# Performance work log

Measured on AMD Instinct MI355X. Metric: run time of the kernel, lower is better.

The kernel has to match this reference:

```python
import jax, jax.numpy as jnp
import numpy as np

IN_FEATURES = 4096
OUT_FEATURES = 4096
BANDWIDTH = min(IN_FEATURES, OUT_FEATURES) // 8  # 512, as in the torch default


def band_indices(n_out, n_in, bw):
    """Vectorized equivalent of BandMatrix.create_band_indices (COO row/col lists)."""
    i = np.arange(n_out)
    lo = np.maximum(0, i - bw)
    hi = np.minimum(n_in, i + bw + 1)
    counts = hi - lo
    total = int(counts.sum())
    rows = np.repeat(i, counts)
    start = np.cumsum(counts) - counts  # offset of each row's first entry
    cols = np.arange(total) - np.repeat(start, counts) + np.repeat(lo, counts)
    return rows.astype(np.int32), cols.astype(np.int32)


def setup_inputs() -> dict:
    key = jax.random.key(0)
    kx, kw = jax.random.split(key)
    rows_np, cols_np = band_indices(OUT_FEATURES, IN_FEATURES, BANDWIDTH)
    nnz = rows_np.shape[0]  # 3935744
    x = jax.random.normal(kx, (4, 2048, IN_FEATURES), dtype=jnp.float32)
    W_values = jax.random.normal(kw, (nnz,), dtype=jnp.float32)
    bias = jnp.zeros((OUT_FEATURES,), dtype=jnp.float32)
    return {
        "x": x,
        "W_values": W_values,
        "bias": bias,
        "rows": jnp.asarray(rows_np),
        "cols": jnp.asarray(cols_np),
    }


def reference(x, W_values, bias, rows, cols):
    # Densify banded COO weight [out, in] (matches sparse_coo_tensor().to_dense()).
    W = jnp.zeros((OUT_FEATURES, IN_FEATURES), dtype=W_values.dtype).at[rows, cols].set(W_values)
    # x: [B, S, in] @ W.T: [in, out] -> [B, S, out]
    out = jnp.einsum('bsi,oi->bso', x, W) + bias
    return out
```

## Files before the change

### kernel.cpp

```cpp
#include <hip/hip_runtime.h>
#include <stdint.h>

#define IN_F  4096
#define OUT_F 4096
#define BW    512
#define WB2   1280
#define BM    256
#define BN    256

typedef __bf16 bf16x8 __attribute__((ext_vector_type(8)));
typedef float  f32x4  __attribute__((ext_vector_type(4)));

__device__ __forceinline__ int band_start(int o) {
    if (o <= 512)  return o * 513 + ((o * (o - 1)) >> 1);
    if (o <= 3584) return 393472 + (o - 512) * 1025;
    const int d = o - 3584;
    return 3542272 + (((1024 + 4609 - o) * d) >> 1);
}

__device__ __forceinline__ uint16_t f32_to_bf16(float f) {
    uint32_t u = __builtin_bit_cast(uint32_t, f);
    u += 0x7FFFu + ((u >> 16) & 1u);
    return (uint16_t)(u >> 16);
}

__global__ __launch_bounds__(256) void cvt_x(const float* __restrict__ x,
                                             uint16_t* __restrict__ xb, int n4) {
    const int stride = gridDim.x * 256;
    for (int i = blockIdx.x * 256 + threadIdx.x; i < n4; i += stride) {
        const float4 v = reinterpret_cast<const float4*>(x)[i];
        const uint32_t lo = (uint32_t)f32_to_bf16(v.x) | ((uint32_t)f32_to_bf16(v.y) << 16);
        const uint32_t hi = (uint32_t)f32_to_bf16(v.z) | ((uint32_t)f32_to_bf16(v.w) << 16);
        reinterpret_cast<uint2*>(xb)[i] = make_uint2(lo, hi);
    }
}

__global__ __launch_bounds__(256) void cvt_w(const float* __restrict__ wv,
                                             uint16_t* __restrict__ wd) {
    const int o = blockIdx.y;
    const int j = blockIdx.x * 256 + threadIdx.x;
    const int i = (o & ~(BM - 1)) - BW + j;
    uint16_t v = 0;
    if (i >= o - BW && i <= o + BW && i >= 0 && i < IN_F) {
        const int lo = (o > BW) ? (o - BW) : 0;
        v = f32_to_bf16(wv[band_start(o) + (i - lo)]);
    }
    wd[o * WB2 + j] = v;
}

__global__ __launch_bounds__(512, 1) void band_gemm_v9(
    const uint16_t* __restrict__ xb,
    const uint16_t* __restrict__ wd,
    const float* __restrict__ bias,
    float* __restrict__ out)
{
    __shared__ __align__(128) uint8_t lds[9 * 16384];

    const int id  = blockIdx.x;
    const int xcd = id & 7;
    const int r   = id >> 3;
    const int bx  = 2 * xcd + (r & 1);
    const int by  = r >> 1;
    const int brow = by * BM;
    const int bcol = bx * BN;

    const int wlo    = bcol - BW;
    const int kstart = wlo > 0 ? wlo : 0;
    const int kend   = (bcol + BN + BW) < IN_F ? (bcol + BN + BW) : IN_F;
    const int nt     = (kend - kstart) >> 6;
    const int j0     = kstart - wlo;

    const int tid  = threadIdx.x;
    const int w    = tid >> 6;
    const int lane = tid & 63;
    const int ln   = lane & 15;
    const int kc   = lane >> 4;
    const int wm   = w >> 2;
    const int wn   = w & 3;

    const int srow = tid >> 3;
    const int csrc = (tid & 7) ^ (srow & 7);
    const uint16_t* aSrc = xb + (size_t)(brow + srow) * IN_F + kstart + csrc * 8;
    const uint16_t* bSrc = wd + (size_t)(bcol + srow) * WB2 + j0 + csrc * 8;

#define GLOAD(srcp, dst_off)                                                             \
    __builtin_amdgcn_global_load_lds(                                                    \
        (const __attribute__((address_space(1))) uint32_t*)(srcp),                       \
        (__attribute__((address_space(3))) uint32_t*)(lds + (dst_off) + (w << 10)),      \
        16, 0, 0)

#define STG_UNIT(w_, j_, slot_) {                                                        \
        if (((j_) & 1) == 0) {                                                           \
            const uint16_t* p_ = aSrc + (size_t)(((j_) >> 1) * 128) * IN_F + (w_) * 64;  \
            GLOAD(p_, (slot_) << 14);                                                    \
            GLOAD(p_ + (size_t)64 * IN_F, ((slot_) << 14) + 8192);                       \
        } else {                                                                         \
            const uint16_t* p_ = bSrc + (size_t)(((j_) >> 1) * 128) * WB2 + (w_) * 64;   \
            GLOAD(p_, (slot_) << 14);                                                    \
            GLOAD(p_ + (size_t)64 * WB2, ((slot_) << 14) + 8192);                        \
        } }

    const int cswz = (kc ^ (ln & 7)) << 4;

#define LD_A(BASE, MQ) {                                                                 \
    _Pragma("unroll")                                                                    \
    for (int s_ = 0; s_ < 4; ++s_) {                                                     \
        const int off_ = (BASE) + (((MQ) * 64 + s_ * 16 + ln) << 7) + cswz;              \
        am[s_][0] = *(const bf16x8*)(lds + off_);                                        \
        am[s_][1] = *(const bf16x8*)(lds + (off_ ^ 64));                                 \
    } }
#define LD_B(DST, BASE, NQ) {                                                            \
    _Pragma("unroll")                                                                    \
    for (int s_ = 0; s_ < 2; ++s_) {                                                     \
        const int off_ = (BASE) + (((wn & 1) * 64 + (NQ) * 32 + s_ * 16 + ln) << 7) + cswz; \
        DST[s_][0] = *(const bf16x8*)(lds + off_);                                       \
        DST[s_][1] = *(const bf16x8*)(lds + (off_ ^ 64));                                \
    } }
#define MFMAPH(MROW, NCOL, BB) {                                                         \
    __builtin_amdgcn_s_setprio(1);                                                       \
    _Pragma("unroll")                                                                    \
    for (int a_ = 0; a_ < 4; ++a_) {                                                     \
        _Pragma("unroll")                                                                \
        for (int n_ = 0; n_ < 2; ++n_) {                                                 \
            acc[(MROW) + a_][(NCOL) + n_] = __builtin_amdgcn_mfma_f32_16x16x32_bf16(     \
                am[a_][0], BB[n_][0], acc[(MROW) + a_][(NCOL) + n_], 0, 0, 0);           \
            acc[(MROW) + a_][(NCOL) + n_] = __builtin_amdgcn_mfma_f32_16x16x32_bf16(     \
                am[a_][1], BB[n_][1], acc[(MROW) + a_][(NCOL) + n_], 0, 0, 0);           \
        } }                                                                              \
    __builtin_amdgcn_s_setprio(0); }

    f32x4 acc[8][4] = {};
    bf16x8 am[4][2], bn0[2][2], bn1[2][2];

    STG_UNIT(0, 0, 0); STG_UNIT(0, 1, 1); STG_UNIT(0, 2, 2); STG_UNIT(0, 3, 3);
    STG_UNIT(1, 0, 4);
    asm volatile("s_waitcnt vmcnt(2)" ::: "memory");
    __builtin_amdgcn_s_barrier();

    int s4v = 0;
    for (int v = 0; v < nt; ++v) {
        int sA = s4v + (wm << 1);           if (sA >= 9) sA -= 9;
        int sB = s4v + 1 + ((wn >> 1) << 1); if (sB >= 9) sB -= 9;
        const int aBase = sA << 14, bBase = sB << 14;
        int st0 = s4v + 5; if (st0 >= 9) st0 -= 9;
        int st1 = st0 + 1; if (st1 >= 9) st1 -= 9;
        int st2 = st1 + 1; if (st2 >= 9) st2 -= 9;
        int st3 = st2 + 1; if (st3 >= 9) st3 -= 9;
        const bool stg_q012 = (v + 1 < nt);
        const bool stg_q3   = (v + 2 < nt);

        LD_A(aBase, 0);
        LD_B(bn0, bBase, 0);
        if (stg_q012) STG_UNIT(v + 1, 1, st0);
        MFMAPH(0, 0, bn0);
        LD_B(bn1, bBase, 1);
        if (stg_q012) STG_UNIT(v + 1, 2, st1);
        MFMAPH(0, 2, bn1);
        LD_A(aBase, 1);
        if (stg_q012) STG_UNIT(v + 1, 3, st2);
        MFMAPH(4, 2, bn1);
        if (stg_q3) STG_UNIT(v + 2, 0, st3);
        MFMAPH(4, 0, bn0);

        if (v + 1 < nt) {
            if (v + 2 < nt) { asm volatile("s_waitcnt vmcnt(2)" ::: "memory"); }
            else            { asm volatile("s_waitcnt vmcnt(0)" ::: "memory"); }
            __builtin_amdgcn_s_barrier();
        }
        s4v += 4; if (s4v >= 9) s4v -= 9;
    }
#undef STG_UNIT
#undef GLOAD

    const int ocol = bcol + wn * 64 + ln;
    float bsv[4];
    #pragma unroll
    for (int n = 0; n < 4; ++n) bsv[n] = bias[ocol + n * 16];

    #pragma unroll
    for (int a = 0; a < 8; ++a) {
        #pragma unroll
        for (int q = 0; q < 4; ++q) {
            const int row = brow + wm * 128 + a * 16 + (kc << 2) + q;
            float* po = out + (size_t)row * OUT_F + ocol;
            #pragma unroll
            for (int n = 0; n < 4; ++n)
                po[n * 16] = acc[a][n][q] + bsv[n];
        }
    }
}

__global__ __launch_bounds__(256) void band_gemm_f32(
    const float* __restrict__ x, const float* __restrict__ wv,
    const float* __restrict__ bias, float* __restrict__ out, int M)
{
    __shared__ float Xs[128][33];
    __shared__ float Ws[32][130];
    const int tid = threadIdx.x;
    const int tx = tid & 15, ty = tid >> 4;
    const int bcol = blockIdx.x * 128, brow = blockIdx.y * 128;
    const int klo = (bcol >= BW) ? (bcol - BW) : 0;
    const int khi = min(IN_F, bcol + 128 + BW);
    float acc[8][8];
    #pragma unroll
    for (int a = 0; a < 8; ++a)
        #pragma unroll
        for (int b = 0; b < 8; ++b) acc[a][b] = 0.f;
    const int xc4 = (tid & 7) * 4, xr0 = tid >> 3;
    const int wc = tid & 31, wr0 = tid >> 5;
    for (int k0 = klo; k0 < khi; k0 += 32) {
        #pragma unroll
        for (int p = 0; p < 4; ++p) {
            const int rr = xr0 + 32 * p;
            const float4 v = *reinterpret_cast<const float4*>(&x[(size_t)(brow + rr) * IN_F + (k0 + xc4)]);
            Xs[rr][xc4 + 0] = v.x; Xs[rr][xc4 + 1] = v.y; Xs[rr][xc4 + 2] = v.z; Xs[rr][xc4 + 3] = v.w;
        }
        const int i = k0 + wc;
        #pragma unroll
        for (int p = 0; p < 16; ++p) {
            const int rr = wr0 + 8 * p;
            const int o = bcol + rr;
            const int lo = (o >= BW) ? (o - BW) : 0;
            float v = 0.f;
            if (i >= o - BW && i <= o + BW) v = wv[band_start(o) + (i - lo)];
            Ws[wc][rr] = v;
        }
        __syncthreads();
        #pragma unroll
        for (int k = 0; k < 32; ++k) {
            float amv[8];
            #pragma unroll
            for (int a = 0; a < 8; ++a) amv[a] = Xs[ty * 8 + a][k];
            float bo[8];
            #pragma unroll
            for (int b = 0; b < 4; ++b) { bo[b] = Ws[k][tx * 4 + b]; bo[4 + b] = Ws[k][tx * 4 + 64 + b]; }
            #pragma unroll
            for (int a = 0; a < 8; ++a)
                #pragma unroll
                for (int b = 0; b < 8; ++b) acc[a][b] = fmaf(amv[a], bo[b], acc[a][b]);
        }
        __syncthreads();
    }
    #pragma unroll
    for (int a = 0; a < 8; ++a) {
        const size_t row = (size_t)(brow + ty * 8 + a);
        #pragma unroll
        for (int b = 0; b < 4; ++b) {
            out[row * OUT_F + bcol + tx * 4 + b]      = acc[a][b]     + bias[bcol + tx * 4 + b];
            out[row * OUT_F + bcol + tx * 4 + 64 + b] = acc[a][4 + b] + bias[bcol + tx * 4 + 64 + b];
        }
    }
}

extern "C" void kernel_launch(void* const* d_in, const int* in_sizes, int n_in,
                              void* d_out, int out_size, void* d_ws, size_t ws_size,
                              hipStream_t stream) {
    const float* x    = (const float*)d_in[0];
    const float* wv   = (const float*)d_in[1];
    const float* bias = (const float*)d_in[2];
    float* out        = (float*)d_out;

    const int M = in_sizes[0] / IN_F;
    const size_t xb_bytes = (size_t)M * IN_F * 2;
    const size_t wd_bytes = (size_t)OUT_F * WB2 * 2;

    if (ws_size >= xb_bytes + wd_bytes && (M % BM) == 0) {
        uint16_t* xb  = (uint16_t*)d_ws;
        uint16_t* wdp = (uint16_t*)((uint8_t*)d_ws + xb_bytes);
        cvt_x<<<2048, 256, 0, stream>>>(x, xb, M * IN_F / 4);
        cvt_w<<<dim3(WB2 / 256, OUT_F), 256, 0, stream>>>(wv, wdp);
        band_gemm_v9<<<(M / BM) * (OUT_F / BN), 512, 0, stream>>>(xb, wdp, bias, out);
    } else {
        dim3 grid(OUT_F / 128, M / 128);
        band_gemm_f32<<<grid, 256, 0, stream>>>(x, wv, bias, out, M);
    }
}
```

Measured before the change: 140.4 us.

## Process two row tiles per block to overlap epilogue with next prologue

The GEMM grid shrinks to 256 persistent-style blocks, and each block computes two 256x256 output tiles (row groups byg and byg+16) in sequence. The second tile's prologue global loads are issued before the first tile's epilogue stores, so the store phase hides load latency and one tail wave is removed. It also drops the s_setprio around MFMA phases. The fast path is now hardcoded to M == 8192, and the kernel does twice the serial work per block.

```diff
diff --git a/kernel.cpp b/kernel.cpp
--- a/kernel.cpp
+++ b/kernel.cpp
@@ -48,7 +48,7 @@
     wd[o * WB2 + j] = v;
 }
 
-__global__ __launch_bounds__(512, 1) void band_gemm_v9(
+__global__ __launch_bounds__(512, 1) void band_gemm_v10(
     const uint16_t* __restrict__ xb,
     const uint16_t* __restrict__ wd,
     const float* __restrict__ bias,
@@ -57,12 +57,10 @@
     __shared__ __align__(128) uint8_t lds[9 * 16384];
 
     const int id  = blockIdx.x;
-    const int xcd = id & 7;
-    const int r   = id >> 3;
-    const int bx  = 2 * xcd + (r & 1);
-    const int by  = r >> 1;
-    const int brow = by * BM;
+    const int bx  = 2 * (id & 7) + ((id >> 3) & 1);
+    const int byg = id >> 4;
     const int bcol = bx * BN;
+    const int brow0 = byg * BM;
 
     const int wlo    = bcol - BW;
     const int kstart = wlo > 0 ? wlo : 0;
@@ -80,8 +78,9 @@
 
     const int srow = tid >> 3;
     const int csrc = (tid & 7) ^ (srow & 7);
-    const uint16_t* aSrc = xb + (size_t)(brow + srow) * IN_F + kstart + csrc * 8;
-    const uint16_t* bSrc = wd + (size_t)(bcol + srow) * WB2 + j0 + csrc * 8;
+    const uint16_t* aSrc0 = xb + (size_t)(brow0 + srow) * IN_F + kstart + csrc * 8;
+    const uint16_t* aSrc1 = aSrc0 + (size_t)16 * BM * IN_F;
+    const uint16_t* bSrc  = wd + (size_t)(bcol + srow) * WB2 + j0 + csrc * 8;
 
 #define GLOAD(srcp, dst_off)                                                             \
     __builtin_amdgcn_global_load_lds(                                                    \
@@ -89,9 +88,9 @@
         (__attribute__((address_space(3))) uint32_t*)(lds + (dst_off) + (w << 10)),      \
         16, 0, 0)
 
-#define STG_UNIT(w_, j_, slot_) {                                                        \
+#define STG_UNIT(AS, w_, j_, slot_) {                                                    \
         if (((j_) & 1) == 0) {                                                           \
-            const uint16_t* p_ = aSrc + (size_t)(((j_) >> 1) * 128) * IN_F + (w_) * 64;  \
+            const uint16_t* p_ = (AS) + (size_t)(((j_) >> 1) * 128) * IN_F + (w_) * 64;  \
             GLOAD(p_, (slot_) << 14);                                                    \
             GLOAD(p_ + (size_t)64 * IN_F, ((slot_) << 14) + 8192);                       \
         } else {                                                                         \
@@ -117,7 +116,6 @@
         DST[s_][1] = *(const bf16x8*)(lds + (off_ ^ 64));                                \
     } }
 #define MFMAPH(MROW, NCOL, BB) {                                                         \
-    __builtin_amdgcn_s_setprio(1);                                                       \
     _Pragma("unroll")                                                                    \
     for (int a_ = 0; a_ < 4; ++a_) {                                                     \
         _Pragma("unroll")                                                                \
@@ -126,68 +124,86 @@
                 am[a_][0], BB[n_][0], acc[(MROW) + a_][(NCOL) + n_], 0, 0, 0);           \
             acc[(MROW) + a_][(NCOL) + n_] = __builtin_amdgcn_mfma_f32_16x16x32_bf16(     \
                 am[a_][1], BB[n_][1], acc[(MROW) + a_][(NCOL) + n_], 0, 0, 0);           \
-        } }                                                                              \
-    __builtin_amdgcn_s_setprio(0); }
+        } } }
+
+#define PRO(AS) {                                                                        \
+    STG_UNIT(AS, 0, 0, 0); STG_UNIT(AS, 0, 1, 1); STG_UNIT(AS, 0, 2, 2);                 \
+    STG_UNIT(AS, 0, 3, 3); STG_UNIT(AS, 1, 0, 4); }
+
+#define KLOOP(AS) {                                                                      \
+    int s4v = 0;                                                                         \
+    for (int v = 0; v < nt; ++v) {                                                       \
+        int sA = s4v + (wm << 1);            if (sA >= 9) sA -= 9;                       \
+        int sB = s4v + 1 + ((wn >> 1) << 1); if (sB >= 9) sB -= 9;                       \
+        const int aBase = sA << 14, bBase = sB << 14;                                    \
+        int st0 = s4v + 5; if (st0 >= 9) st0 -= 9;                                       \
+        int st1 = st0 + 1; if (st1 >= 9) st1 -= 9;                                       \
+        int st2 = st1 + 1; if (st2 >= 9) st2 -= 9;                                       \
+        int st3 = st2 + 1; if (st3 >= 9) st3 -= 9;                                       \
+        const bool stg_q012 = (v + 1 < nt);                                              \
+        const bool stg_q3   = (v + 2 < nt);                                              \
+        LD_A(aBase, 0);                                                                  \
+        LD_B(bn0, bBase, 0);                                                             \
+        if (stg_q012) STG_UNIT(AS, v + 1, 1, st0);                                       \
+        MFMAPH(0, 0, bn0);                                                               \
+        LD_B(bn1, bBase, 1);                                                             \
+        if (stg_q012) STG_UNIT(AS, v + 1, 2, st1);                                       \
+        MFMAPH(0, 2, bn1);                                                               \
+        LD_A(aBase, 1);                                                                  \
+        if (stg_q012) STG_UNIT(AS, v + 1, 3, st2);                                       \
+        MFMAPH(4, 2, bn1);                                                               \
+        if (stg_q3) STG_UNIT(AS, v + 2, 0, st3);                                         \
+        MFMAPH(4, 0, bn0);                                                               \
+        if (v + 1 < nt) {                                                                \
+            if (v + 2 < nt) { asm volatile("s_waitcnt vmcnt(2)" ::: "memory"); }         \
+            else            { asm volatile("s_waitcnt vmcnt(0)" ::: "memory"); }         \
+            __builtin_amdgcn_s_barrier();                                                \
+        }                                                                                \
+        s4v += 4; if (s4v >= 9) s4v -= 9;                                                \
+    } }
+
+#define EPI(BROWX) {                                                                     \
+    _Pragma("unroll")                                                                    \
+    for (int a_ = 0; a_ < 8; ++a_) {                                                     \
+        _Pragma("unroll")                                                                \
+        for (int q_ = 0; q_ < 4; ++q_) {                                                 \
+            const int row_ = (BROWX) + wm * 128 + a_ * 16 + (kc << 2) + q_;              \
+            float* po_ = out + (size_t)row_ * OUT_F + ocol;                              \
+            _Pragma("unroll")                                                            \
+            for (int n_ = 0; n_ < 4; ++n_)                                               \
+                po_[n_ * 16] = acc[a_][n_][q_] + bsv[n_];                                 \
+        } } }
+
+    const int ocol = bcol + wn * 64 + ln;
+    float bsv[4];
+    #pragma unroll
+    for (int n = 0; n < 4; ++n) bsv[n] = bias[ocol + n * 16];
 
     f32x4 acc[8][4] = {};
     bf16x8 am[4][2], bn0[2][2], bn1[2][2];
 
-    STG_UNIT(0, 0, 0); STG_UNIT(0, 1, 1); STG_UNIT(0, 2, 2); STG_UNIT(0, 3, 3);
-    STG_UNIT(1, 0, 4);
+    PRO(aSrc0);
     asm volatile("s_waitcnt vmcnt(2)" ::: "memory");
     __builtin_amdgcn_s_barrier();
-
-    int s4v = 0;
-    for (int v = 0; v < nt; ++v) {
-        int sA = s4v + (wm << 1);           if (sA >= 9) sA -= 9;
-        int sB = s4v + 1 + ((wn >> 1) << 1); if (sB >= 9) sB -= 9;
-        const int aBase = sA << 14, bBase = sB << 14;
-        int st0 = s4v + 5; if (st0 >= 9) st0 -= 9;
-        int st1 = st0 + 1; if (st1 >= 9) st1 -= 9;
-        int st2 = st1 + 1; if (st2 >= 9) st2 -= 9;
-        int st3 = st2 + 1; if (st3 >= 9) st3 -= 9;
-        const bool stg_q012 = (v + 1 < nt);
-        const bool stg_q3   = (v + 2 < nt);
-
-        LD_A(aBase, 0);
-        LD_B(bn0, bBase, 0);
-        if (stg_q012) STG_UNIT(v + 1, 1, st0);
-        MFMAPH(0, 0, bn0);
-        LD_B(bn1, bBase, 1);
-        if (stg_q012) STG_UNIT(v + 1, 2, st1);
-        MFMAPH(0, 2, bn1);
-        LD_A(aBase, 1);
-        if (stg_q012) STG_UNIT(v + 1, 3, st2);
-        MFMAPH(4, 2, bn1);
-        if (stg_q3) STG_UNIT(v + 2, 0, st3);
-        MFMAPH(4, 0, bn0);
-
-        if (v + 1 < nt) {
-            if (v + 2 < nt) { asm volatile("s_waitcnt vmcnt(2)" ::: "memory"); }
-            else            { asm volatile("s_waitcnt vmcnt(0)" ::: "memory"); }
-            __builtin_amdgcn_s_barrier();
-        }
-        s4v += 4; if (s4v >= 9) s4v -= 9;
-    }
+    KLOOP(aSrc0);
+    __builtin_amdgcn_s_barrier();
+
+    PRO(aSrc1);
+    asm volatile("s_waitcnt vmcnt(2)" ::: "memory");
+    __builtin_amdgcn_s_barrier();
+    EPI(brow0);
+    #pragma unroll
+    for (int a = 0; a < 8; ++a)
+        #pragma unroll
+        for (int n = 0; n < 4; ++n) acc[a][n] = (f32x4){0.f, 0.f, 0.f, 0.f};
+    KLOOP(aSrc1);
+    EPI(brow0 + 16 * BM);
+
 #undef STG_UNIT
 #undef GLOAD
-
-    const int ocol = bcol + wn * 64 + ln;
-    float bsv[4];
-    #pragma unroll
-    for (int n = 0; n < 4; ++n) bsv[n] = bias[ocol + n * 16];
-
-    #pragma unroll
-    for (int a = 0; a < 8; ++a) {
-        #pragma unroll
-        for (int q = 0; q < 4; ++q) {
-            const int row = brow + wm * 128 + a * 16 + (kc << 2) + q;
-            float* po = out + (size_t)row * OUT_F + ocol;
-            #pragma unroll
-            for (int n = 0; n < 4; ++n)
-                po[n * 16] = acc[a][n][q] + bsv[n];
-        }
-    }
+#undef PRO
+#undef KLOOP
+#undef EPI
 }
 
 __global__ __launch_bounds__(256) void band_gemm_f32(
@@ -264,12 +280,12 @@
     const size_t xb_bytes = (size_t)M * IN_F * 2;
     const size_t wd_bytes = (size_t)OUT_F * WB2 * 2;
 
-    if (ws_size >= xb_bytes + wd_bytes && (M % BM) == 0) {
+    if (ws_size >= xb_bytes + wd_bytes && M == 8192) {
         uint16_t* xb  = (uint16_t*)d_ws;
         uint16_t* wdp = (uint16_t*)((uint8_t*)d_ws + xb_bytes);
         cvt_x<<<2048, 256, 0, stream>>>(x, xb, M * IN_F / 4);
         cvt_w<<<dim3(WB2 / 256, OUT_F), 256, 0, stream>>>(wv, wdp);
-        band_gemm_v9<<<(M / BM) * (OUT_F / BN), 512, 0, stream>>>(xb, wdp, bias, out);
+        band_gemm_v10<<<256, 512, 0, stream>>>(xb, wdp, bias, out);
     } else {
         dim3 grid(OUT_F / 128, M / 128);
         band_gemm_f32<<<grid, 256, 0, stream>>>(x, wv, bias, out, M);
```

After: 139.3 us. About the same (-0.8%).
